# Kernel tuning notes

Hardware: AMD Instinct MI355X
Metric: run time of the kernel (lower is better)

The kernel has to match this reference:

```python
import jax, jax.numpy as jnp
import numpy as np

B, S, DIM = 16, 1024, 1024
GAMMA = 0.96875
EPS = 1e-3  # keras GroupNormalization default epsilon


def setup_inputs() -> dict:
    key = jax.random.key(0)
    ks = jax.random.split(key, 4)
    scale = 1.0 / np.sqrt(DIM)
    return {
        "x": jax.random.normal(ks[0], (B, S, DIM), dtype=jnp.float32),
        "Wq": jax.random.normal(ks[1], (DIM, DIM), dtype=jnp.float32) * scale,
        "Wk": jax.random.normal(ks[2], (DIM, DIM), dtype=jnp.float32) * scale,
        "Wv": jax.random.normal(ks[3], (DIM, DIM), dtype=jnp.float32) * scale,
        "gn_scale": jnp.ones((DIM,), dtype=jnp.float32),
        "gn_beta": jnp.zeros((DIM,), dtype=jnp.float32),
    }


def reference(x, Wq, Wk, Wv, gn_scale, gn_beta):
    # Bias-free projections
    Q = x @ Wq  # [B,S,D]
    K = x @ Wk
    V = x @ Wv
    # Full (non-causal) exponential decay matrix D[i,j] = gamma^(i-j)
    idx = jnp.arange(S, dtype=jnp.float32)
    D = GAMMA ** (idx[:, None] - idx[None, :])  # [S,S]
    scores = jnp.einsum("bsd,btd->bst", Q, K) * D  # [B,S,S]
    y = scores @ V  # [B,S,D]
    # GroupNorm with groups == channels: normalize each channel over seq axis
    mean = jnp.mean(y, axis=1, keepdims=True)  # [B,1,D]
    var = jnp.var(y, axis=1, keepdims=True)
    y_hat = (y - mean) * jax.lax.rsqrt(var + EPS)
    return y_hat * gn_scale + gn_beta
```

## Files before the change

### kernel.cpp

```cpp
#include <hip/hip_runtime.h>
#include <cmath>

#define BATCH_ 16
#define SN_ 1024
#define DN_ 1024

constexpr float EPS_ = 1e-3f;

typedef unsigned short ushort;
typedef __attribute__((ext_vector_type(8))) short short8;
typedef __attribute__((ext_vector_type(8))) unsigned short ushort8;
typedef __attribute__((ext_vector_type(16))) float f32x16;

__device__ __forceinline__ ushort f2b(float f) {
    unsigned u = __float_as_uint(f);
    unsigned r = (u + 0x7fffu + ((u >> 16) & 1u)) >> 16;
    return (ushort)r;
}

__device__ __forceinline__ void gload16(const void* g, void* l) {
    __builtin_amdgcn_global_load_lds(
        (const __attribute__((address_space(1))) void*)g,
        (__attribute__((address_space(3))) void*)l, 16, 0, 0);
}

#define SCHED0 __builtin_amdgcn_sched_barrier(0)
#define MFMA32(a, b, c) __builtin_amdgcn_mfma_f32_32x32x16_bf16(a, b, c, 0, 0, 0)

template<int MODE>
__global__ __launch_bounds__(512, 2)
void gemm_bf(const ushort* __restrict__ A0, const ushort* __restrict__ B0,
             void* __restrict__ C0, void* __restrict__ C1, void* __restrict__ C2,
             float* __restrict__ psum, float* __restrict__ psq,
             long sA, long sB, long sBm, long sC, float coef)
{
    __shared__ __align__(16) char lds[131072];

    const int gx = gridDim.x, gy = gridDim.y;
    int lid   = blockIdx.x + gx * (blockIdx.y + gy * blockIdx.z);
    int total = gx * gy * gridDim.z;
    int swz   = (lid & 7) * (total >> 3) + (lid >> 3);
    int bx = swz % gx;
    int rest = swz / gx;
    int by = rest % gy;
    int bz = rest / gy;

    const int m0 = by * 256, n0 = bx * 256;
    const ushort* A  = A0 + (long)bz * sA;
    const ushort* Bp = B0 + (long)bz * sB + (long)(m0 >> 10) * sBm;

    const int t = threadIdx.x;
    const int l = t & 63, w = t >> 6;
    const int wr = w >> 2, wc = w & 3;
    const int ln = l & 31;
    const int kb = l >> 5;
    const int lx = l & 7;

    const int aOff = (wr * 128 + ln) * 128;
    const int bOff = 32768 + (wc * 64 + ln) * 128;

    const int rl   = t >> 3;
    const int slot = (t & 7) ^ (rl & 7);
    const ushort* gA = A  + (long)(m0 + rl) * 1024 + slot * 8;
    const ushort* gB = Bp + (long)(n0 + rl) * 1024 + slot * 8;
    char* lA = lds + t * 16;
    char* lB = lds + 32768 + t * 16;

#define STA(h, k0, bo_) gload16(gA + (long)(h) * 65536 + (k0), lA + (bo_) + (h) * 8192)
#define STB(h, k0, bo_) gload16(gB + (long)(h) * 65536 + (k0), lB + (bo_) + (h) * 8192)

    f32x16 acc[4][2] = {};

    STB(0, 0, 0); STB(1, 0, 0); STB(2, 0, 0); STB(3, 0, 0);
    STA(0, 0, 0); STA(1, 0, 0); STA(2, 0, 0); STA(3, 0, 0);
    SCHED0;
    asm volatile("s_waitcnt vmcnt(0)" ::: "memory");
    SCHED0;
    __builtin_amdgcn_s_barrier();
    SCHED0;

    for (int kt = 0; kt < 16; ++kt) {
        const int bo = (kt & 1) << 16;
        const int bn = bo ^ 65536;
        const int k1 = (kt + 1) << 6;
        const bool st = kt < 15;
        const char* base = lds + bo;

#pragma unroll
        for (int p = 0; p < 4; ++p) {
            const int sxp = ((p * 2 + kb) ^ lx) * 16;
            short8 a0 = *(const short8*)(base + aOff + 0 * 4096 + sxp);
            short8 a1 = *(const short8*)(base + aOff + 1 * 4096 + sxp);
            short8 a2 = *(const short8*)(base + aOff + 2 * 4096 + sxp);
            short8 a3 = *(const short8*)(base + aOff + 3 * 4096 + sxp);
            short8 b0 = *(const short8*)(base + bOff + 0 * 4096 + sxp);
            short8 b1 = *(const short8*)(base + bOff + 1 * 4096 + sxp);
            if (st) {
                if (p == 0) { STB(0, k1, bn); STB(1, k1, bn);
                              STB(2, k1, bn); STB(3, k1, bn); }
                else if (p == 1) { STA(0, k1, bn); STA(1, k1, bn);
                                   STA(2, k1, bn); STA(3, k1, bn); }
            }
            __builtin_amdgcn_s_setprio(1);
            acc[0][0] = MFMA32(a0, b0, acc[0][0]);
            acc[0][1] = MFMA32(a0, b1, acc[0][1]);
            acc[1][0] = MFMA32(a1, b0, acc[1][0]);
            acc[1][1] = MFMA32(a1, b1, acc[1][1]);
            acc[2][0] = MFMA32(a2, b0, acc[2][0]);
            acc[2][1] = MFMA32(a2, b1, acc[2][1]);
            acc[3][0] = MFMA32(a3, b0, acc[3][0]);
            acc[3][1] = MFMA32(a3, b1, acc[3][1]);
            __builtin_amdgcn_s_setprio(0);
            SCHED0;
        }
        asm volatile("s_waitcnt vmcnt(0)" ::: "memory");
        SCHED0;
        __builtin_amdgcn_s_barrier();
        SCHED0;
    }

    if constexpr (MODE == 4) {
        ushort* C = (ushort*)C0 + (long)bz * sC;
#pragma unroll
        for (int mi = 0; mi < 4; ++mi)
#pragma unroll
            for (int reg = 0; reg < 16; ++reg) {
                int row = m0 + wr * 128 + mi * 32 + (reg & 3) + 8 * (reg >> 2) + 4 * kb;
#pragma unroll
                for (int nj = 0; nj < 2; ++nj)
                    C[(long)row * 1024 + n0 + wc * 64 + nj * 32 + ln] =
                        f2b(acc[mi][nj][reg]);
            }
    } else if constexpr (MODE == 5) {
        ushort* C = (ushort*)C0;
        float cs0 = 0.f, cq0 = 0.f, cs1 = 0.f, cq1 = 0.f;
#pragma unroll
        for (int mi = 0; mi < 4; ++mi)
#pragma unroll
            for (int reg = 0; reg < 16; ++reg) {
                float v0 = acc[mi][0][reg], v1 = acc[mi][1][reg];
                cs0 += v0; cq0 += v0 * v0;
                cs1 += v1; cq1 += v1 * v1;
                int row = m0 + wr * 128 + mi * 32 + (reg & 3) + 8 * (reg >> 2) + 4 * kb;
                C[(long)row * 1024 + n0 + wc * 64 + ln]      = f2b(v0);
                C[(long)row * 1024 + n0 + wc * 64 + 32 + ln] = f2b(v1);
            }
        float* S4 = (float*)lds;
        float* Q4 = (float*)(lds + 4096);
        {
            int c0i = wc * 64 + ln, c1i = wc * 64 + 32 + ln, idx = wr * 2 + kb;
            S4[c0i * 4 + idx] = cs0; S4[c1i * 4 + idx] = cs1;
            Q4[c0i * 4 + idx] = cq0; Q4[c1i * 4 + idx] = cq1;
        }
        __syncthreads();
        if (t < 256) {
            float s = S4[t * 4] + S4[t * 4 + 1] + S4[t * 4 + 2] + S4[t * 4 + 3];
            float q = Q4[t * 4] + Q4[t * 4 + 1] + Q4[t * 4 + 2] + Q4[t * 4 + 3];
            psum[(long)by * 1024 + n0 + t] = s;
            psq [(long)by * 1024 + n0 + t] = q;
        }
    } else {
        const int which = n0 >> 10;
        const int nq = n0 & 1023;
        if (which == 0) {
            ushort* C = (ushort*)C0;
#pragma unroll
            for (int mi = 0; mi < 4; ++mi)
#pragma unroll
                for (int reg = 0; reg < 16; ++reg) {
                    int row = m0 + wr * 128 + mi * 32 + (reg & 3) + 8 * (reg >> 2) + 4 * kb;
                    float s = exp2f(coef * (float)(row & 1023));
#pragma unroll
                    for (int nj = 0; nj < 2; ++nj)
                        C[(long)row * 1024 + nq + wc * 64 + nj * 32 + ln] =
                            f2b(acc[mi][nj][reg] * s);
                }
        } else {
            ushort* Tl = (ushort*)lds;
            const int bb = m0 >> 10;
            const int ms = m0 & 1023;
            ushort* Ct = (ushort*)((which == 1) ? C1 : C2) + (long)bb * sC;
            const float cf = (which == 1) ? -coef : 0.0f;
            __syncthreads();
#pragma unroll
            for (int mi = 0; mi < 4; ++mi)
#pragma unroll
                for (int reg = 0; reg < 16; ++reg) {
                    int rm = wr * 128 + mi * 32 + (reg & 3) + 8 * (reg >> 2) + 4 * kb;
                    float s = exp2f(cf * (float)(ms + rm));
#pragma unroll
                    for (int nj = 0; nj < 2; ++nj) {
                        int cn = wc * 64 + nj * 32 + ln;
                        int p  = (rm >> 3) ^ (cn & 31);
                        Tl[cn * 256 + p * 8 + (rm & 7)] = f2b(acc[mi][nj][reg] * s);
                    }
                }
            __syncthreads();
#pragma unroll
            for (int it = 0; it < 16; ++it) {
                int cn = (t >> 5) + it * 16;
                int ch = t & 31;
                int p  = ch ^ (cn & 31);
                ushort8 v = *(const ushort8*)&Tl[cn * 256 + p * 8];
                *(ushort8*)&Ct[(long)(nq + cn) * 1024 + ms + ch * 8] = v;
            }
        }
    }
#undef STA
#undef STB
}

__global__ __launch_bounds__(256)
void conv_x_k(const float* __restrict__ x, ushort* __restrict__ xb)
{
    long i = ((long)blockIdx.x * 256 + threadIdx.x) * 8;
    float4 a = *(const float4*)&x[i];
    float4 b = *(const float4*)&x[i + 4];
    ushort8 v;
    v[0] = f2b(a.x); v[1] = f2b(a.y); v[2] = f2b(a.z); v[3] = f2b(a.w);
    v[4] = f2b(b.x); v[5] = f2b(b.y); v[6] = f2b(b.z); v[7] = f2b(b.w);
    *(ushort8*)&xb[i] = v;
}

__global__ __launch_bounds__(256)
void wt_k(const float* __restrict__ W, ushort* __restrict__ Wt)
{
    __shared__ float Tl[32][33];
    int tx = threadIdx.x & 31, ty = threadIdx.x >> 5;
    int c0 = blockIdx.x * 32, r0 = blockIdx.y * 32;
#pragma unroll
    for (int i = 0; i < 4; i++)
        Tl[ty + 8 * i][tx] = W[(long)(r0 + ty + 8 * i) * 1024 + c0 + tx];
    __syncthreads();
#pragma unroll
    for (int i = 0; i < 4; i++)
        Wt[(long)(c0 + ty + 8 * i) * 1024 + r0 + tx] = f2b(Tl[tx][ty + 8 * i]);
}

__global__ __launch_bounds__(256)
void stats2(const float* __restrict__ psum, const float* __restrict__ psq,
            const float* __restrict__ gsc, const float* __restrict__ gbt,
            float* __restrict__ fs, float* __restrict__ bias)
{
    int d = blockIdx.x * 256 + threadIdx.x;
    int b = blockIdx.y;
    float s = 0.f, q = 0.f;
#pragma unroll
    for (int z = 0; z < 4; z++) {
        long o = ((long)(b * 4 + z) << 10) + d;
        s += psum[o];
        q += psq[o];
    }
    float mean = s * (1.0f / SN_);
    float var  = q * (1.0f / SN_) - mean * mean;
    var = fmaxf(var, 0.0f);
    float rstd = rsqrtf(var + EPS_);
    float f = rstd * gsc[d];
    fs[(long)b * DN_ + d]   = f;
    bias[(long)b * DN_ + d] = gbt[d] - mean * f;
}

__global__ __launch_bounds__(256)
void norm_k(const ushort* __restrict__ yb, const float* __restrict__ fs,
            const float* __restrict__ bias, float* __restrict__ out)
{
    long i = ((long)blockIdx.x * 256 + threadIdx.x) * 8;
    int d = (int)(i & (DN_ - 1));
    int b = (int)(i >> 20);
    ushort8 v = *(const ushort8*)&yb[i];
    long o = (long)b * DN_ + d;
    float4 f0 = *(const float4*)&fs[o];
    float4 f1 = *(const float4*)&fs[o + 4];
    float4 b0 = *(const float4*)&bias[o];
    float4 b1 = *(const float4*)&bias[o + 4];
    float4 o0, o1;
    o0.x = __uint_as_float((unsigned)v[0] << 16) * f0.x + b0.x;
    o0.y = __uint_as_float((unsigned)v[1] << 16) * f0.y + b0.y;
    o0.z = __uint_as_float((unsigned)v[2] << 16) * f0.z + b0.z;
    o0.w = __uint_as_float((unsigned)v[3] << 16) * f0.w + b0.w;
    o1.x = __uint_as_float((unsigned)v[4] << 16) * f1.x + b1.x;
    o1.y = __uint_as_float((unsigned)v[5] << 16) * f1.y + b1.y;
    o1.z = __uint_as_float((unsigned)v[6] << 16) * f1.z + b1.z;
    o1.w = __uint_as_float((unsigned)v[7] << 16) * f1.w + b1.w;
    *(float4*)&out[i]     = o0;
    *(float4*)&out[i + 4] = o1;
}

extern "C" void kernel_launch(void* const* d_in, const int* in_sizes, int n_in,
                              void* d_out, int out_size, void* d_ws, size_t ws_size,
                              hipStream_t stream)
{
    const float* x   = (const float*)d_in[0];
    const float* Wq  = (const float*)d_in[1];
    const float* Wk  = (const float*)d_in[2];
    const float* Wv  = (const float*)d_in[3];
    const float* gsc = (const float*)d_in[4];
    const float* gbt = (const float*)d_in[5];
    float* out = (float*)d_out;

    const long SD = (long)SN_ * DN_;
    const long DD = (long)DN_ * DN_;
    const size_t MB32 = (size_t)SD * BATCH_ * sizeof(ushort);

    char* ws = (char*)d_ws;
    ushort* xb  = (ushort*)(ws);
    ushort* Qp  = (ushort*)(ws + 1 * MB32);
    ushort* Kt  = (ushort*)(ws + 2 * MB32);
    ushort* Vt  = (ushort*)(ws + 3 * MB32);
    ushort* Mt  = (ushort*)(ws + 4 * MB32);
    ushort* Wct = (ushort*)(ws + 5 * MB32);
    float*  psum = (float*)(ws + 5 * MB32 + (6u << 20));
    float*  psq  = (float*)(ws + 5 * MB32 + (6u << 20) + (1u << 18));
    float*  fs   = (float*)(ws + 5 * MB32 + (6u << 20) + (2u << 18));
    float*  bias = (float*)(ws + 5 * MB32 + (6u << 20) + (2u << 18) + (1u << 16));
    ushort* yb  = xb;

    const float lgf = (float)log2(0.96875);

    dim3 blk512(512);
    dim3 blk(256);
    dim3 gproj(12, 64);
    dim3 gmt(4, 4, 16);
    dim3 gy(4, 64);

    conv_x_k<<<dim3(8192), blk, 0, stream>>>(x, xb);
    wt_k<<<dim3(32, 32), blk, 0, stream>>>(Wq, Wct);
    wt_k<<<dim3(32, 32), blk, 0, stream>>>(Wk, Wct + 1024 * 1024);
    wt_k<<<dim3(32, 32), blk, 0, stream>>>(Wv, Wct + 2 * 1024 * 1024);

    gemm_bf<6><<<gproj, blk512, 0, stream>>>(xb, Wct, Qp, Kt, Vt,
                                             nullptr, nullptr,
                                             0, 0, 0, SD, lgf);
    gemm_bf<4><<<gmt, blk512, 0, stream>>>(Vt, Kt, Mt, nullptr, nullptr,
                                           nullptr, nullptr,
                                           SD, SD, 0, DD, 0.0f);
    gemm_bf<5><<<gy, blk512, 0, stream>>>(Qp, Mt, yb, nullptr, nullptr,
                                          psum, psq,
                                          0, 0, DD, 0, 0.0f);

    stats2<<<dim3(4, 16), blk, 0, stream>>>(psum, psq, gsc, gbt, fs, bias);
    norm_k<<<dim3(8192), blk, 0, stream>>>(yb, fs, bias, out);
}
```

Baseline: 237.9 us.

## Use 1024-thread GEMM blocks with 16 waves each owning a 64x64 sub-tile

Doubles the GEMM block from 8 to 16 waves on the same 256x256 tile, so each wave holds a 64x64 accumulator instead of 128x64. Per-thread global-to-LDS staging loads drop from eight to four, and the stats reduction now sums eight partials. The transpose epilogue packs four bf16 values into one vector LDS store instead of scalar stores. The aim is more waves to hide latency and lower register pressure, at the cost of fewer MFMAs per LDS fragment load and more LDS read traffic per FLOP.

Result: faster. 232.7 us (-2.2%).

```diff
diff --git a/kernel.cpp b/kernel.cpp
--- a/kernel.cpp
+++ b/kernel.cpp
@@ -8,6 +8,7 @@
 constexpr float EPS_ = 1e-3f;
 
 typedef unsigned short ushort;
+typedef __attribute__((ext_vector_type(4))) unsigned short ushort4_t;
 typedef __attribute__((ext_vector_type(8))) short short8;
 typedef __attribute__((ext_vector_type(8))) unsigned short ushort8;
 typedef __attribute__((ext_vector_type(16))) float f32x16;
@@ -28,7 +29,7 @@
 #define MFMA32(a, b, c) __builtin_amdgcn_mfma_f32_32x32x16_bf16(a, b, c, 0, 0, 0)
 
 template<int MODE>
-__global__ __launch_bounds__(512, 2)
+__global__ __launch_bounds__(1024, 4)
 void gemm_bf(const ushort* __restrict__ A0, const ushort* __restrict__ B0,
              void* __restrict__ C0, void* __restrict__ C1, void* __restrict__ C2,
              float* __restrict__ psum, float* __restrict__ psq,
@@ -56,7 +57,7 @@
     const int kb = l >> 5;
     const int lx = l & 7;
 
-    const int aOff = (wr * 128 + ln) * 128;
+    const int aOff = (wr * 64 + ln) * 128;
     const int bOff = 32768 + (wc * 64 + ln) * 128;
 
     const int rl   = t >> 3;
@@ -66,13 +67,12 @@
     char* lA = lds + t * 16;
     char* lB = lds + 32768 + t * 16;
 
-#define STA(h, k0, bo_) gload16(gA + (long)(h) * 65536 + (k0), lA + (bo_) + (h) * 8192)
-#define STB(h, k0, bo_) gload16(gB + (long)(h) * 65536 + (k0), lB + (bo_) + (h) * 8192)
-
-    f32x16 acc[4][2] = {};
-
-    STB(0, 0, 0); STB(1, 0, 0); STB(2, 0, 0); STB(3, 0, 0);
-    STA(0, 0, 0); STA(1, 0, 0); STA(2, 0, 0); STA(3, 0, 0);
+#define STA(h, k0, bo_) gload16(gA + (long)(h) * 131072 + (k0), lA + (bo_) + (h) * 16384)
+#define STB(h, k0, bo_) gload16(gB + (long)(h) * 131072 + (k0), lB + (bo_) + (h) * 16384)
+
+    f32x16 acc[2][2] = {};
+
+    STA(0, 0, 0); STA(1, 0, 0); STB(0, 0, 0); STB(1, 0, 0);
     SCHED0;
     asm volatile("s_waitcnt vmcnt(0)" ::: "memory");
     SCHED0;
@@ -91,25 +91,17 @@
             const int sxp = ((p * 2 + kb) ^ lx) * 16;
             short8 a0 = *(const short8*)(base + aOff + 0 * 4096 + sxp);
             short8 a1 = *(const short8*)(base + aOff + 1 * 4096 + sxp);
-            short8 a2 = *(const short8*)(base + aOff + 2 * 4096 + sxp);
-            short8 a3 = *(const short8*)(base + aOff + 3 * 4096 + sxp);
             short8 b0 = *(const short8*)(base + bOff + 0 * 4096 + sxp);
             short8 b1 = *(const short8*)(base + bOff + 1 * 4096 + sxp);
             if (st) {
-                if (p == 0) { STB(0, k1, bn); STB(1, k1, bn);
-                              STB(2, k1, bn); STB(3, k1, bn); }
-                else if (p == 1) { STA(0, k1, bn); STA(1, k1, bn);
-                                   STA(2, k1, bn); STA(3, k1, bn); }
+                if (p == 0) { STA(0, k1, bn); STA(1, k1, bn); }
+                else if (p == 1) { STB(0, k1, bn); STB(1, k1, bn); }
             }
             __builtin_amdgcn_s_setprio(1);
             acc[0][0] = MFMA32(a0, b0, acc[0][0]);
             acc[0][1] = MFMA32(a0, b1, acc[0][1]);
             acc[1][0] = MFMA32(a1, b0, acc[1][0]);
             acc[1][1] = MFMA32(a1, b1, acc[1][1]);
-            acc[2][0] = MFMA32(a2, b0, acc[2][0]);
-            acc[2][1] = MFMA32(a2, b1, acc[2][1]);
-            acc[3][0] = MFMA32(a3, b0, acc[3][0]);
-            acc[3][1] = MFMA32(a3, b1, acc[3][1]);
             __builtin_amdgcn_s_setprio(0);
             SCHED0;
         }
@@ -122,10 +114,10 @@
     if constexpr (MODE == 4) {
         ushort* C = (ushort*)C0 + (long)bz * sC;
 #pragma unroll
-        for (int mi = 0; mi < 4; ++mi)
+        for (int mi = 0; mi < 2; ++mi)
 #pragma unroll
             for (int reg = 0; reg < 16; ++reg) {
-                int row = m0 + wr * 128 + mi * 32 + (reg & 3) + 8 * (reg >> 2) + 4 * kb;
+                int row = m0 + wr * 64 + mi * 32 + (reg & 3) + 8 * (reg >> 2) + 4 * kb;
 #pragma unroll
                 for (int nj = 0; nj < 2; ++nj)
                     C[(long)row * 1024 + n0 + wc * 64 + nj * 32 + ln] =
@@ -135,27 +127,28 @@
         ushort* C = (ushort*)C0;
         float cs0 = 0.f, cq0 = 0.f, cs1 = 0.f, cq1 = 0.f;
 #pragma unroll
-        for (int mi = 0; mi < 4; ++mi)
+        for (int mi = 0; mi < 2; ++mi)
 #pragma unroll
             for (int reg = 0; reg < 16; ++reg) {
                 float v0 = acc[mi][0][reg], v1 = acc[mi][1][reg];
                 cs0 += v0; cq0 += v0 * v0;
                 cs1 += v1; cq1 += v1 * v1;
-                int row = m0 + wr * 128 + mi * 32 + (reg & 3) + 8 * (reg >> 2) + 4 * kb;
+                int row = m0 + wr * 64 + mi * 32 + (reg & 3) + 8 * (reg >> 2) + 4 * kb;
                 C[(long)row * 1024 + n0 + wc * 64 + ln]      = f2b(v0);
                 C[(long)row * 1024 + n0 + wc * 64 + 32 + ln] = f2b(v1);
             }
         float* S4 = (float*)lds;
-        float* Q4 = (float*)(lds + 4096);
+        float* Q4 = (float*)(lds + 8192);
         {
             int c0i = wc * 64 + ln, c1i = wc * 64 + 32 + ln, idx = wr * 2 + kb;
-            S4[c0i * 4 + idx] = cs0; S4[c1i * 4 + idx] = cs1;
-            Q4[c0i * 4 + idx] = cq0; Q4[c1i * 4 + idx] = cq1;
+            S4[c0i * 8 + idx] = cs0; S4[c1i * 8 + idx] = cs1;
+            Q4[c0i * 8 + idx] = cq0; Q4[c1i * 8 + idx] = cq1;
         }
         __syncthreads();
         if (t < 256) {
-            float s = S4[t * 4] + S4[t * 4 + 1] + S4[t * 4 + 2] + S4[t * 4 + 3];
-            float q = Q4[t * 4] + Q4[t * 4 + 1] + Q4[t * 4 + 2] + Q4[t * 4 + 3];
+            float s = 0.f, q = 0.f;
+#pragma unroll
+            for (int z = 0; z < 8; ++z) { s += S4[t * 8 + z]; q += Q4[t * 8 + z]; }
             psum[(long)by * 1024 + n0 + t] = s;
             psq [(long)by * 1024 + n0 + t] = q;
         }
@@ -165,10 +158,10 @@
         if (which == 0) {
             ushort* C = (ushort*)C0;
 #pragma unroll
-            for (int mi = 0; mi < 4; ++mi)
+            for (int mi = 0; mi < 2; ++mi)
 #pragma unroll
                 for (int reg = 0; reg < 16; ++reg) {
-                    int row = m0 + wr * 128 + mi * 32 + (reg & 3) + 8 * (reg >> 2) + 4 * kb;
+                    int row = m0 + wr * 64 + mi * 32 + (reg & 3) + 8 * (reg >> 2) + 4 * kb;
                     float s = exp2f(coef * (float)(row & 1023));
 #pragma unroll
                     for (int nj = 0; nj < 2; ++nj)
@@ -183,22 +176,29 @@
             const float cf = (which == 1) ? -coef : 0.0f;
             __syncthreads();
 #pragma unroll
-            for (int mi = 0; mi < 4; ++mi)
-#pragma unroll
-                for (int reg = 0; reg < 16; ++reg) {
-                    int rm = wr * 128 + mi * 32 + (reg & 3) + 8 * (reg >> 2) + 4 * kb;
-                    float s = exp2f(cf * (float)(ms + rm));
+            for (int mi = 0; mi < 2; ++mi)
+#pragma unroll
+                for (int g = 0; g < 4; ++g) {
+                    int rq = wr * 8 + mi * 4 + g;
+                    int rb = 8 * g + 4 * kb;
 #pragma unroll
                     for (int nj = 0; nj < 2; ++nj) {
                         int cn = wc * 64 + nj * 32 + ln;
-                        int p  = (rm >> 3) ^ (cn & 31);
-                        Tl[cn * 256 + p * 8 + (rm & 7)] = f2b(acc[mi][nj][reg] * s);
+                        int p  = rq ^ (cn & 31);
+                        ushort4_t u;
+#pragma unroll
+                        for (int e = 0; e < 4; ++e) {
+                            int rm = wr * 64 + mi * 32 + rb + e;
+                            float s = exp2f(cf * (float)(ms + rm));
+                            u[e] = f2b(acc[mi][nj][g * 4 + e] * s);
+                        }
+                        *(ushort4_t*)&Tl[cn * 256 + p * 8 + 4 * kb] = u;
                     }
                 }
             __syncthreads();
 #pragma unroll
-            for (int it = 0; it < 16; ++it) {
-                int cn = (t >> 5) + it * 16;
+            for (int it = 0; it < 8; ++it) {
+                int cn = (t >> 5) + it * 32;
                 int ch = t & 31;
                 int p  = ch ^ (cn & 31);
                 ushort8 v = *(const ushort8*)&Tl[cn * 256 + p * 8];
@@ -317,7 +317,7 @@
 
     const float lgf = (float)log2(0.96875);
 
-    dim3 blk512(512);
+    dim3 blk1k(1024);
     dim3 blk(256);
     dim3 gproj(12, 64);
     dim3 gmt(4, 4, 16);
@@ -328,15 +328,15 @@
     wt_k<<<dim3(32, 32), blk, 0, stream>>>(Wk, Wct + 1024 * 1024);
     wt_k<<<dim3(32, 32), blk, 0, stream>>>(Wv, Wct + 2 * 1024 * 1024);
 
-    gemm_bf<6><<<gproj, blk512, 0, stream>>>(xb, Wct, Qp, Kt, Vt,
-                                             nullptr, nullptr,
-                                             0, 0, 0, SD, lgf);
-    gemm_bf<4><<<gmt, blk512, 0, stream>>>(Vt, Kt, Mt, nullptr, nullptr,
-                                           nullptr, nullptr,
-                                           SD, SD, 0, DD, 0.0f);
-    gemm_bf<5><<<gy, blk512, 0, stream>>>(Qp, Mt, yb, nullptr, nullptr,
-                                          psum, psq,
-                                          0, 0, DD, 0, 0.0f);
+    gemm_bf<6><<<gproj, blk1k, 0, stream>>>(xb, Wct, Qp, Kt, Vt,
+                                            nullptr, nullptr,
+                                            0, 0, 0, SD, lgf);
+    gemm_bf<4><<<gmt, blk1k, 0, stream>>>(Vt, Kt, Mt, nullptr, nullptr,
+                                          nullptr, nullptr,
+                                          SD, SD, 0, DD, 0.0f);
+    gemm_bf<5><<<gy, blk1k, 0, stream>>>(Qp, Mt, yb, nullptr, nullptr,
+                                         psum, psq,
+                                         0, 0, DD, 0, 0.0f);
 
     stats2<<<dim3(4, 16), blk, 0, stream>>>(psum, psq, gsc, gbt, fs, bias);
     norm_k<<<dim3(8192), blk, 0, stream>>>(yb, fs, bias, out);
```
